# Kernel optimization log

Hardware: AMD Instinct MI355X
Metric: run time of the kernel (lower is better)

The kernel has to match this reference:

```python
import jax, jax.numpy as jnp
import numpy as np

L = 2        # rnn_num_layer
H = 512      # rnn_hidden_size
E = 512      # embed_dim == rnn_input_size
B = 16
T_DEC = 512
S_ENC = 512
VOCAB = 1001 # num_embed
OUT = 1000   # output_size
PAD = 0.0


def setup_inputs() -> dict:
    key = jax.random.key(0)
    ks = jax.random.split(key, 16)
    s = 0.05
    trg_inputs = jax.random.randint(ks[0], (B, T_DEC), 0, VOCAB)
    trg_len = jnp.clip(jax.random.randint(ks[1], (B,), 0, T_DEC + 1), 1, T_DEC)
    encoder_outputs = jax.random.normal(ks[2], (B, S_ENC, H), dtype=jnp.float32)
    h0 = jax.random.normal(ks[3], (L * 2, B, H), dtype=jnp.float32)
    c0 = jax.random.normal(ks[4], (L * 2, B, H), dtype=jnp.float32)
    embed = jax.random.normal(ks[5], (VOCAB, E)) * s
    W_ih0 = jax.random.normal(ks[6], (2, 4 * H, E)) * s          # layer 0, fwd/bwd dirs
    W_ih1 = jax.random.normal(ks[7], (L - 1, 2, 4 * H, 2 * H)) * s  # layers>0 take concat(fwd,bwd)
    W_hh = jax.random.normal(ks[8], (L, 2, 4 * H, H)) * s
    b_ih = jax.random.normal(ks[9], (L, 2, 4 * H)) * s
    b_hh = jax.random.normal(ks[10], (L, 2, 4 * H)) * s
    W_att = jax.random.normal(ks[11], (H, H)) * s  # Attention 'general' linear
    b_att = jax.random.normal(ks[12], (H,)) * s
    W_fc = jax.random.normal(ks[13], (OUT, 2 * H)) * s
    b_fc = jax.random.normal(ks[14], (OUT,)) * s
    return dict(trg_inputs=trg_inputs, trg_len=trg_len, encoder_outputs=encoder_outputs,
                h0=h0, c0=c0, embed=embed, W_ih0=W_ih0, W_ih1=W_ih1, W_hh=W_hh,
                b_ih=b_ih, b_hh=b_hh, W_att=W_att, b_att=b_att, W_fc=W_fc, b_fc=b_fc)


def _cell(x, h, c, Wi, Wh, bi, bh):
    # PyTorch LSTM gate order: i, f, g, o
    g = x @ Wi.T + h @ Wh.T + bi + bh  # [B, 4H]
    i, f, gg, o = jnp.split(g, 4, axis=-1)
    c2 = jax.nn.sigmoid(f) * c + jax.nn.sigmoid(i) * jnp.tanh(gg)
    h2 = jax.nn.sigmoid(o) * jnp.tanh(c2)
    return h2, c2


def _decode(trg_inputs, trg_len, encoder_outputs, h0, c0, embed,
            W_ih0, W_ih1, W_hh, b_ih, b_hh, W_att, b_att, W_fc, b_fc):
    Bb, T = trg_inputs.shape
    S = encoder_outputs.shape[1]
    # 'general' attention projection of encoder outputs (hoisted out of the loop)
    enc_proj = jnp.einsum('bsh,gh->bsg', encoder_outputs, W_att) + b_att
    enc_mask = jnp.arange(S)[None, :] < trg_len[:, None]          # [B, S]
    step_valid = jnp.arange(T)[:, None] < trg_len[None, :]        # [T, B]
    h = h0.reshape(L, 2, Bb, H)
    c = c0.reshape(L, 2, Bb, H)

    def step(carry, xt):
        h, c = carry
        tok, valid = xt                                           # [B], [B]
        xin = embed[tok]                                          # [B, E]
        hs, cs = [], []
        for l in range(L):
            Wi = W_ih0 if l == 0 else W_ih1[l - 1]
            hf, cf = _cell(xin, h[l, 0], c[l, 0], Wi[0], W_hh[l, 0], b_ih[l, 0], b_hh[l, 0])
            hb, cb = _cell(xin, h[l, 1], c[l, 1], Wi[1], W_hh[l, 1], b_ih[l, 1], b_hh[l, 1])
            hs.append(jnp.stack([hf, hb]))
            cs.append(jnp.stack([cf, cb]))
            xin = jnp.concatenate([hf, hb], axis=-1)              # input to next layer [B, 2H]
        h2 = jnp.stack(hs)
        c2 = jnp.stack(cs)
        dec = hs[-1][0] + hs[-1][1]                               # sum fwd+bwd halves [B, H]
        score = jnp.einsum('bh,bsh->bs', dec, enc_proj)
        score = jnp.where(enc_mask, score, -1e30)                 # ragged length mask
        att = jax.nn.softmax(score, axis=-1)
        ctx = jnp.einsum('bs,bsh->bh', att, encoder_outputs)
        fc = jnp.concatenate([dec, ctx], axis=-1) @ W_fc.T + b_fc # [B, OUT]
        out = jnp.where(valid[:, None], fc, PAD)                  # positions past trg_len stay pad
        return (h2, c2), out

    _, outs = jax.lax.scan(step, (h, c), (trg_inputs.T, step_valid))
    return outs.transpose(1, 0, 2)                                # [B, T, OUT]


def reference(trg_inputs, trg_len, encoder_outputs, h0, c0, embed,
              W_ih0, W_ih1, W_hh, b_ih, b_hh, W_att, b_att, W_fc, b_fc):
    return _decode(trg_inputs, trg_len, encoder_outputs, h0, c0, embed,
                   W_ih0, W_ih1, W_hh, b_ih, b_hh, W_att, b_att, W_fc, b_fc)
```

## Files before the change

kernel.cpp:

```cpp
#include <hip/hip_runtime.h>
#include <cstdint>
#include <cstddef>

typedef __attribute__((ext_vector_type(8))) short short8;
typedef __attribute__((ext_vector_type(4))) float f32x4;
typedef __attribute__((ext_vector_type(4))) unsigned int uint4v;

#define DEV static __device__ __forceinline__

DEV float b2f(unsigned short u){ union{unsigned int i; float f;} v; v.i = ((unsigned int)u)<<16; return v.f; }
DEV unsigned short f2b(float f){
  union{float f; unsigned int i;} v; v.f = f;
  unsigned int u = v.i;
  unsigned int r = (u + 0x7fffu + ((u>>16)&1u)) >> 16;
  return (unsigned short)r;
}
DEV float sigm(float x){ return 1.0f/(1.0f + __expf(-x)); }
DEV float tanhfast(float x){ return 1.0f - 2.0f/(1.0f + __expf(2.0f*x)); }

DEV uint4v ld_sc_b128(const unsigned short* p){
  uint4v d;
  asm volatile("global_load_dwordx4 %0, %1, off sc0 sc1" : "=v"(d) : "v"(p) : "memory");
  return d;
}
DEV short8 ldw8(const float* p){
  short8 w;
  #pragma unroll
  for (int e = 0; e < 8; ++e) w[e] = (short)f2b(p[e]);
  return w;
}

__global__ __launch_bounds__(256) void k_cast(const float* __restrict__ s, unsigned short* __restrict__ d, int n){
  int i = blockIdx.x*256 + threadIdx.x;
  if (i < n) d[i] = f2b(s[i]);
}
__global__ __launch_bounds__(256) void k_transpose_enc(const float* __restrict__ enc, unsigned short* __restrict__ encT){
  int i = blockIdx.x*256 + threadIdx.x;
  if (i >= 16*512*512) return;
  int b = i >> 18, r = i & 262143, h = r >> 9, s = r & 511;
  encT[i] = f2b(enc[(b<<18) + (s<<9) + h]);
}
__global__ __launch_bounds__(256) void k_gather(const int* __restrict__ trg, const float* __restrict__ emb, unsigned short* __restrict__ X){
  int i = blockIdx.x*256 + threadIdx.x;
  if (i >= 8192*512) return;
  int r = i >> 9, e = i & 511;
  int t = r >> 4, b = r & 15;
  int tok = trg[(b<<9) + t];
  X[i] = f2b(emb[((size_t)tok<<9) + e]);
}
__global__ __launch_bounds__(256) void k_bsum(const float* __restrict__ bi, const float* __restrict__ bh, float* __restrict__ o){
  int i = blockIdx.x*256 + threadIdx.x;
  if (i < 8192) o[i] = bi[i] + bh[i];
}
__global__ __launch_bounds__(256) void k_init(const float* __restrict__ h0, unsigned short* __restrict__ Hst0,
                                              unsigned short* __restrict__ Hst1, unsigned int* __restrict__ bar){
  int i = blockIdx.x*256 + threadIdx.x;
  if (i < 256) bar[i] = 0;
  if (i < 16384) {
    Hst0[i] = f2b(h0[i]);
    Hst1[i] = f2b(h0[16384 + i]);
  }
}
__global__ __launch_bounds__(256) void k_split(const float* __restrict__ S, unsigned short* __restrict__ E3, int n){
  int i = blockIdx.x*256 + threadIdx.x;
  if (i >= n) return;
  int r = i >> 9, j = i & 511;
  float f = S[i];
  unsigned short hi = f2b(f);
  unsigned short lo = f2b(f - b2f(hi));
  size_t base = (size_t)r * 1536 + j;
  E3[base] = hi;
  E3[base + 512] = lo;
  E3[base + 1024] = hi;
}
__global__ __launch_bounds__(256) void k_decsplit(const float* __restrict__ HF, unsigned short* __restrict__ DCTX,
                                                  unsigned short* __restrict__ D3){
  int i = blockIdx.x*256 + threadIdx.x;
  if (i >= 8192*512) return;
  int r = i >> 9, j = i & 511;
  float d = HF[((size_t)r<<10) + j] + HF[((size_t)r<<10) + 512 + j];
  unsigned short hi = f2b(d);
  unsigned short lo = f2b(d - b2f(hi));
  DCTX[((size_t)r<<10) + j] = hi;
  size_t base = (size_t)r * 1536 + j;
  D3[base] = hi;
  D3[base + 512] = hi;
  D3[base + 1024] = lo;
}

template<int MODE>
__global__ __launch_bounds__(256) void k_gemm(
    const unsigned short* __restrict__ A, long lda, long sA,
    const unsigned short* __restrict__ W, long ldw, long sW,
    void* __restrict__ C, long ldc, long sC,
    const float* __restrict__ bias,
    int M, int N, int K,
    const int* __restrict__ tlen)
{
  __shared__ short8 AsV[128*5];
  __shared__ short8 WsV[128*5];
  const int bz = blockIdx.z;
  const unsigned short* Ab = A + (size_t)bz * sA;
  const unsigned short* Wb = W + (size_t)bz * sW;
  const int m0 = blockIdx.x << 7, n0 = blockIdx.y << 7;
  const int tid = threadIdx.x;
  const int wave = tid >> 6, lane = tid & 63;
  const int ln = lane & 15, kq = lane >> 4;
  const int wm = wave >> 1, wn = wave & 1;
  const int ar0 = tid >> 2, ac0 = (tid & 3) << 3;
  const int ar1 = ar0 + 64;
  const short8 z8 = {0,0,0,0,0,0,0,0};

  f32x4 acc[4][4];
  #pragma unroll
  for (int i = 0; i < 4; ++i)
    #pragma unroll
    for (int j = 0; j < 4; ++j) { f32x4 z = {0.f,0.f,0.f,0.f}; acc[i][j] = z; }

  for (int k0 = 0; k0 < K; k0 += 32) {
    short8 a0 = *(const short8*)(Ab + (size_t)(m0+ar0)*lda + k0 + ac0);
    short8 a1 = *(const short8*)(Ab + (size_t)(m0+ar1)*lda + k0 + ac0);
    short8 w0 = z8, w1 = z8;
    if (MODE != 2 || (n0+ar0) < N) w0 = *(const short8*)(Wb + (size_t)(n0+ar0)*ldw + k0 + ac0);
    if (MODE != 2 || (n0+ar1) < N) w1 = *(const short8*)(Wb + (size_t)(n0+ar1)*ldw + k0 + ac0);
    __syncthreads();
    AsV[ar0*5 + (ac0>>3)] = a0;
    AsV[ar1*5 + (ac0>>3)] = a1;
    WsV[ar0*5 + (ac0>>3)] = w0;
    WsV[ar1*5 + (ac0>>3)] = w1;
    __syncthreads();
    short8 af[4], wf[4];
    #pragma unroll
    for (int i = 0; i < 4; ++i) af[i] = AsV[((wm<<6) + (i<<4) + ln)*5 + kq];
    #pragma unroll
    for (int i = 0; i < 4; ++i) wf[i] = WsV[((wn<<6) + (i<<4) + ln)*5 + kq];
    #pragma unroll
    for (int i = 0; i < 4; ++i)
      #pragma unroll
      for (int j = 0; j < 4; ++j)
        acc[i][j] = __builtin_amdgcn_mfma_f32_16x16x32_bf16(af[i], wf[j], acc[i][j], 0, 0, 0);
  }
  #pragma unroll
  for (int j = 0; j < 4; ++j) {
    const int n = n0 + (wn<<6) + (j<<4) + ln;
    float bi = 0.f;
    if (MODE == 0 || MODE == 1) { if (bias) bi = bias[n]; }
    if (MODE == 2) { if (n < N) bi = bias[n]; }
    #pragma unroll
    for (int i = 0; i < 4; ++i) {
      #pragma unroll
      for (int r = 0; r < 4; ++r) {
        const int m = m0 + (wm<<6) + (i<<4) + (kq<<2) + r;
        float v = acc[i][j][r] + bi;
        if (MODE == 0) ((unsigned short*)C)[(size_t)bz*sC + (size_t)m*ldc + n] = f2b(v);
        else if (MODE == 1) ((float*)C)[(size_t)bz*sC + (size_t)m*ldc + n] = v;
        else {
          if (n < N) {
            int tt = m >> 4, bb = m & 15;
            ((float*)C)[((size_t)((bb<<9) + tt))*1000 + n] = (tt < tlen[bb]) ? v : 0.0f;
          }
        }
      }
    }
  }
}

__global__ __launch_bounds__(256, 1) void k_recur(
    const float* __restrict__ whh,
    const float* __restrict__ wih1,
    const unsigned short* __restrict__ Xg0,
    const float* __restrict__ c0all,
    const float* __restrict__ bsum,
    unsigned short* __restrict__ Hst0,
    unsigned short* __restrict__ Hst1,
    unsigned short* __restrict__ Hcat,
    float* __restrict__ HcatF,
    unsigned int* __restrict__ flags)
{
  const int bid = blockIdx.x;
  const int dir = (bid >> 5) & 1;
  const int j0  = (bid & 31) << 4;
  const int tid = threadIdx.x;
  const int wave = tid >> 6, lane = tid & 63;
  const int ln = lane & 15, kq = lane >> 4;
  const int b_ = tid >> 4, jl = tid & 15;
  const int myfl = bid & 31, pollfl = lane & 31;

  __shared__ __align__(16) unsigned char h0sh[32768];
  __shared__ __align__(16) unsigned char h1sh[16384];
  __shared__ float gsh[4][16][16];

  unsigned int* FL0d0 = flags;
  unsigned int* FL0d1 = flags + 32;

  if (bid < 64) {
    unsigned int* FL = flags + (dir << 5);
    short8 wfrag[16];
    {
      const float* wb = whh + (((size_t)((dir<<11) + (wave<<9) + j0 + ln)) << 9) + (kq<<3);
      #pragma unroll
      for (int ks = 0; ks < 16; ++ks) wfrag[ks] = ldw8(wb + (ks<<5));
    }
    float c = c0all[(((size_t)((dir<<4) + b_)) << 9) + j0 + jl];

    size_t xr = ((size_t)b_ << 12) + (dir<<11) + j0 + jl;
    float xg0 = b2f(Xg0[xr]);
    float xg1 = b2f(Xg0[xr + 512]);
    float xg2 = b2f(Xg0[xr + 1024]);
    float xg3 = b2f(Xg0[xr + 1536]);

    for (int t = 0; t < 512; ++t) {
      const unsigned short* hbase = Hst0 + ((((t&1)<<1) + dir)<<13);
      uint4v st[4];
      #pragma unroll
      for (int cc = 0; cc < 4; ++cc)
        st[cc] = ld_sc_b128(hbase + (cc<<11) + (tid<<3));
      asm volatile("s_waitcnt vmcnt(0)" ::: "memory");
      #pragma unroll
      for (int cc = 0; cc < 4; ++cc) {
        int g = (cc<<8) + tid, row = g >> 6, slot = g & 63, ps = slot ^ row;
        *(uint4v*)(h1sh + row*1024 + (ps<<4)) = st[cc];
      }
      __syncthreads();

      f32x4 acc0 = {0.f,0.f,0.f,0.f}, acc1 = {0.f,0.f,0.f,0.f};
      #pragma unroll
      for (int ks = 0; ks < 16; ks += 2) {
        short8 a0 = *(const short8*)(h1sh + ln*1024 + ((((ks<<2)+kq) ^ ln)<<4));
        short8 a1 = *(const short8*)(h1sh + ln*1024 + (((((ks+1)<<2)+kq) ^ ln)<<4));
        acc0 = __builtin_amdgcn_mfma_f32_16x16x32_bf16(a0, wfrag[ks],   acc0, 0, 0, 0);
        acc1 = __builtin_amdgcn_mfma_f32_16x16x32_bf16(a1, wfrag[ks+1], acc1, 0, 0, 0);
      }
      f32x4 acc = acc0 + acc1;
      #pragma unroll
      for (int r = 0; r < 4; ++r)
        gsh[wave][(kq<<2)+r][ln] = acc[r];
      __syncthreads();

      float gi = gsh[0][b_][jl] + xg0;
      float gf = gsh[1][b_][jl] + xg1;
      float gg = gsh[2][b_][jl] + xg2;
      float go = gsh[3][b_][jl] + xg3;
      float ii = sigm(gi), ff = sigm(gf);
      float g2 = tanhfast(gg), oo = sigm(go);
      c = ff*c + ii*g2;
      float h = oo * tanhfast(c);
      unsigned short h16 = f2b(h);

      unsigned int hu = (unsigned int)h16;
      unsigned int hv1 = __shfl_down(hu, 1);
      unsigned int hv2 = __shfl_down(hu, 2);
      unsigned int hv3 = __shfl_down(hu, 3);
      if (!(lane & 3)) {
        unsigned long long hq = (unsigned long long)(hu | (hv1 << 16))
                              | ((unsigned long long)(hv2 | (hv3 << 16)) << 32);
        unsigned short* dst = Hst0 + (((((t+1)&1)<<1) + dir)<<13) + (b_<<9) + j0 + jl;
        __hip_atomic_store((unsigned long long*)dst, hq, __ATOMIC_RELAXED, __HIP_MEMORY_SCOPE_AGENT);
        unsigned short* dc = Hcat + (((size_t)((t<<4) + b_))<<10) + (dir<<9) + j0 + jl;
        __hip_atomic_store((unsigned long long*)dc, hq, __ATOMIC_RELAXED, __HIP_MEMORY_SCOPE_AGENT);
      }

      if (t < 511) {
        xr = (((size_t)(((t+1)<<4) + b_)) << 12) + (dir<<11) + j0 + jl;
        xg0 = b2f(Xg0[xr]);
        xg1 = b2f(Xg0[xr + 512]);
        xg2 = b2f(Xg0[xr + 1024]);
        xg3 = b2f(Xg0[xr + 1536]);
      }

      __syncthreads();
      if (tid == 0)
        __hip_atomic_store(FL + myfl, (unsigned int)(t + 1), __ATOMIC_RELAXED, __HIP_MEMORY_SCOPE_AGENT);
      if (t == 511) break;

      if (wave == 0) {
        const unsigned int tgt = (unsigned int)(t + 1);
        while (!__all((int)(__hip_atomic_load(FL + pollfl, __ATOMIC_RELAXED, __HIP_MEMORY_SCOPE_AGENT) >= tgt)))
          __builtin_amdgcn_s_sleep(1);
      }
      __syncthreads();
    }
  } else {
    unsigned int* FL = flags + 64 + (dir << 5);
    short8 whf[16];
    {
      const float* wb = whh + 2097152 + (((size_t)((dir<<11) + (wave<<9) + j0 + ln)) << 9) + (kq<<3);
      #pragma unroll
      for (int ks = 0; ks < 16; ++ks) whf[ks] = ldw8(wb + (ks<<5));
    }
    short8 wxf[32];
    {
      const float* xb = wih1 + (((size_t)((dir<<11) + (wave<<9) + j0 + ln)) << 10) + (kq<<3);
      #pragma unroll
      for (int ks = 0; ks < 32; ++ks) wxf[ks] = ldw8(xb + (ks<<5));
    }
    float c = c0all[16384 + (((size_t)((dir<<4) + b_)) << 9) + j0 + jl];
    float bs0 = bsum[4096 + (dir<<11) + 0*512 + j0 + jl];
    float bs1 = bsum[4096 + (dir<<11) + 1*512 + j0 + jl];
    float bs2 = bsum[4096 + (dir<<11) + 2*512 + j0 + jl];
    float bs3 = bsum[4096 + (dir<<11) + 3*512 + j0 + jl];

    if (wave == 0) {
      const unsigned int* fp = (lane < 32) ? (FL0d0 + lane) : (FL0d1 + (lane - 32));
      while (!__all((int)(__hip_atomic_load(fp, __ATOMIC_RELAXED, __HIP_MEMORY_SCOPE_AGENT) >= 2u)))
        __builtin_amdgcn_s_sleep(1);
    }
    __syncthreads();

    uint4v sxr[8];
    #pragma unroll
    for (int cc = 0; cc < 8; ++cc) {
      int g = (cc<<8) + tid, row = g >> 7, slot = g & 127;
      sxr[cc] = ld_sc_b128(Hcat + (row<<10) + (slot<<3));
    }
    asm volatile("s_waitcnt vmcnt(0)" ::: "memory");
    #pragma unroll
    for (int cc = 0; cc < 8; ++cc) {
      int g = (cc<<8) + tid, row = g >> 7, slot = g & 127, ps = slot ^ row;
      *(uint4v*)(h0sh + row*2048 + (ps<<4)) = sxr[cc];
    }
    __syncthreads();
    f32x4 xacc;
    {
      f32x4 xa = {0.f,0.f,0.f,0.f}, xb2 = {0.f,0.f,0.f,0.f};
      #pragma unroll
      for (int ks = 0; ks < 32; ks += 2) {
        short8 a0 = *(const short8*)(h0sh + ln*2048 + ((((ks<<2)+kq) ^ ln)<<4));
        short8 a1 = *(const short8*)(h0sh + ln*2048 + (((((ks+1)<<2)+kq) ^ ln)<<4));
        xa  = __builtin_amdgcn_mfma_f32_16x16x32_bf16(a0, wxf[ks],   xa, 0, 0, 0);
        xb2 = __builtin_amdgcn_mfma_f32_16x16x32_bf16(a1, wxf[ks+1], xb2, 0, 0, 0);
      }
      xacc = xa + xb2;
    }
    #pragma unroll
    for (int cc = 0; cc < 8; ++cc) {
      int g = (cc<<8) + tid, row = g >> 7, slot = g & 127;
      sxr[cc] = ld_sc_b128(Hcat + 16384 + (row<<10) + (slot<<3));
    }

    for (int t = 0; t < 512; ++t) {
      if (wave == 0) {
        const unsigned int tgt = (unsigned int)t;
        if (t > 0)
          while (!__all((int)(__hip_atomic_load(FL + pollfl, __ATOMIC_RELAXED, __HIP_MEMORY_SCOPE_AGENT) >= tgt)))
            __builtin_amdgcn_s_sleep(1);
      } else if (wave == 1) {
        const unsigned int tgt = (t + 3 < 512) ? (unsigned int)(t + 3) : 512u;
        const unsigned int* fp = (lane < 32) ? (FL0d0 + lane) : (FL0d1 + (lane - 32));
        while (!__all((int)(__hip_atomic_load(fp, __ATOMIC_RELAXED, __HIP_MEMORY_SCOPE_AGENT) >= tgt)))
          __builtin_amdgcn_s_sleep(1);
      }
      __syncthreads();

      const unsigned short* h1base = Hst1 + ((((t&1)<<1) + dir)<<13);
      uint4v sh[4];
      #pragma unroll
      for (int cc = 0; cc < 4; ++cc)
        sh[cc] = ld_sc_b128(h1base + (cc<<11) + (tid<<3));
      asm volatile("s_waitcnt vmcnt(0)" ::: "memory");
      #pragma unroll
      for (int cc = 0; cc < 4; ++cc) {
        int g = (cc<<8) + tid, row = g >> 6, slot = g & 63, ps = slot ^ row;
        *(uint4v*)(h1sh + row*1024 + (ps<<4)) = sh[cc];
      }
      __syncthreads();

      f32x4 acc0 = xacc, acc1 = {0.f,0.f,0.f,0.f};
      #pragma unroll
      for (int ks = 0; ks < 16; ks += 2) {
        short8 a0 = *(const short8*)(h1sh + ln*1024 + ((((ks<<2)+kq) ^ ln)<<4));
        short8 a1 = *(const short8*)(h1sh + ln*1024 + (((((ks+1)<<2)+kq) ^ ln)<<4));
        acc0 = __builtin_amdgcn_mfma_f32_16x16x32_bf16(a0, whf[ks],   acc0, 0, 0, 0);
        acc1 = __builtin_amdgcn_mfma_f32_16x16x32_bf16(a1, whf[ks+1], acc1, 0, 0, 0);
      }
      f32x4 acc = acc0 + acc1;
      #pragma unroll
      for (int r = 0; r < 4; ++r)
        gsh[wave][(kq<<2)+r][ln] = acc[r];
      __syncthreads();

      float gi = gsh[0][b_][jl] + bs0;
      float gf = gsh[1][b_][jl] + bs1;
      float gg = gsh[2][b_][jl] + bs2;
      float go = gsh[3][b_][jl] + bs3;
      float ii = sigm(gi), ff = sigm(gf);
      float g2 = tanhfast(gg), oo = sigm(go);
      c = ff*c + ii*g2;
      float h = oo * tanhfast(c);
      unsigned short h16 = f2b(h);

      unsigned int hu = (unsigned int)h16;
      unsigned int hv1 = __shfl_down(hu, 1);
      unsigned int hv2 = __shfl_down(hu, 2);
      unsigned int hv3 = __shfl_down(hu, 3);
      if (!(lane & 3)) {
        unsigned long long hq = (unsigned long long)(hu | (hv1 << 16))
                              | ((unsigned long long)(hv2 | (hv3 << 16)) << 32);
        unsigned short* dst = Hst1 + (((((t+1)&1)<<1) + dir)<<13) + (b_<<9) + j0 + jl;
        __hip_atomic_store((unsigned long long*)dst, hq, __ATOMIC_RELAXED, __HIP_MEMORY_SCOPE_AGENT);
      }

      __syncthreads();
      if (tid == 0)
        __hip_atomic_store(FL + myfl, (unsigned int)(t + 1), __ATOMIC_RELAXED, __HIP_MEMORY_SCOPE_AGENT);

      __builtin_nontemporal_store(h, HcatF + (((size_t)((t<<4) + b_))<<10) + (dir<<9) + j0 + jl);

      if (t == 511) break;

      #pragma unroll
      for (int cc = 0; cc < 8; ++cc) {
        int g = (cc<<8) + tid, row = g >> 7, slot = g & 127, ps = slot ^ row;
        *(uint4v*)(h0sh + row*2048 + (ps<<4)) = sxr[cc];
      }
      __syncthreads();
      {
        f32x4 xa = {0.f,0.f,0.f,0.f}, xb2 = {0.f,0.f,0.f,0.f};
        #pragma unroll
        for (int ks = 0; ks < 32; ks += 2) {
          short8 a0 = *(const short8*)(h0sh + ln*2048 + ((((ks<<2)+kq) ^ ln)<<4));
          short8 a1 = *(const short8*)(h0sh + ln*2048 + (((((ks+1)<<2)+kq) ^ ln)<<4));
          xa  = __builtin_amdgcn_mfma_f32_16x16x32_bf16(a0, wxf[ks],   xa, 0, 0, 0);
          xb2 = __builtin_amdgcn_mfma_f32_16x16x32_bf16(a1, wxf[ks+1], xb2, 0, 0, 0);
        }
        xacc = xa + xb2;
      }
      if (t < 510) {
        const unsigned short* hb0 = Hcat + (((size_t)(t+2)) << 14);
        #pragma unroll
        for (int cc = 0; cc < 8; ++cc) {
          int g = (cc<<8) + tid, row = g >> 7, slot = g & 127;
          sxr[cc] = ld_sc_b128(hb0 + (row<<10) + (slot<<3));
        }
      }
    }
  }
}

__global__ __launch_bounds__(256) void k_softmax(const float* __restrict__ score, const int* __restrict__ tlen,
                                                 unsigned short* __restrict__ att){
  int row = (blockIdx.x<<2) + (threadIdx.x>>6);
  int lane = threadIdx.x & 63;
  int b = row >> 9;
  int len = tlen[b];
  const float* sr = score + ((size_t)row<<9);
  float v[8]; float m = -3.0e38f;
  #pragma unroll
  for (int i = 0; i < 8; ++i) {
    int s = (i<<6) + lane;
    float x = sr[s];
    v[i] = (s < len) ? x : -1.0e30f;
    m = fmaxf(m, v[i]);
  }
  #pragma unroll
  for (int off = 32; off; off >>= 1) m = fmaxf(m, __shfl_xor(m, off));
  float sum = 0.f; float p[8];
  #pragma unroll
  for (int i = 0; i < 8; ++i) { p[i] = __expf(v[i] - m); sum += p[i]; }
  #pragma unroll
  for (int off = 32; off; off >>= 1) sum += __shfl_xor(sum, off);
  float inv = 1.0f / sum;
  unsigned short* ar = att + ((size_t)row<<9);
  #pragma unroll
  for (int i = 0; i < 8; ++i) ar[(i<<6) + lane] = f2b(p[i]*inv);
}

extern "C" void kernel_launch(void* const* d_in, const int* in_sizes, int n_in,
                              void* d_out, int out_size, void* d_ws, size_t ws_size,
                              hipStream_t stream) {
  (void)in_sizes; (void)n_in; (void)out_size; (void)ws_size;
  const int*   trg  = (const int*)d_in[0];
  const int*   tlen = (const int*)d_in[1];
  const float* enc  = (const float*)d_in[2];
  const float* h0   = (const float*)d_in[3];
  const float* c0   = (const float*)d_in[4];
  const float* emb  = (const float*)d_in[5];
  const float* wih0 = (const float*)d_in[6];
  const float* wih1 = (const float*)d_in[7];
  const float* whh  = (const float*)d_in[8];
  const float* bih  = (const float*)d_in[9];
  const float* bhh  = (const float*)d_in[10];
  const float* watt = (const float*)d_in[11];
  const float* batt = (const float*)d_in[12];
  const float* wfc  = (const float*)d_in[13];
  const float* bfc  = (const float*)d_in[14];
  float* out = (float*)d_out;

  char* ws = (char*)d_ws;
  size_t off = 0;
  auto alloc = [&](size_t bytes)->char* {
    char* p = ws + off; off += (bytes + 255) & ~(size_t)255; return p;
  };
  unsigned int*   BAR   = (unsigned int*)  alloc(1024);
  unsigned short* XEMB  = (unsigned short*)alloc(8192ll*512*2);
  unsigned short* WI0B  = (unsigned short*)alloc(4096ll*512*2);
  unsigned short* WFCB  = (unsigned short*)alloc(1000ll*1024*2);
  unsigned short* WATTB = (unsigned short*)alloc(512ll*512*2);
  unsigned short* ENCB  = (unsigned short*)alloc(8192ll*512*2);
  unsigned short* ENCT  = (unsigned short*)alloc(8192ll*512*2);
  float*          BSUM  = (float*)         alloc(8192*4);
  unsigned short* HST0  = (unsigned short*)alloc(32768*2);
  unsigned short* HST1  = (unsigned short*)alloc(32768*2);
  unsigned short* XG    = (unsigned short*)alloc(8192ll*4096*2);
  unsigned short* HCAT  = (unsigned short*)alloc(8192ll*1024*2);
  float*          HCATF = (float*)         alloc(8192ll*1024*4);
  float*          SCORE = (float*)         alloc(8192ll*512*4);
  unsigned short* ATT   = (unsigned short*)alloc(8192ll*512*2);
  unsigned short* DCTX  = (unsigned short*)alloc(8192ll*1024*2);
  unsigned short* DEC3  = XG;
  unsigned short* ENC3  = XG + 8192ll*1536;

  auto cdiv = [](long a, long b){ return (int)((a + b - 1) / b); };

  k_cast<<<cdiv(2097152,256),256,0,stream>>>(wih0, WI0B, 2097152);
  k_cast<<<cdiv(1024000,256),256,0,stream>>>(wfc,  WFCB, 1024000);
  k_cast<<<cdiv(262144,256),256,0,stream>>>(watt, WATTB, 262144);
  k_cast<<<cdiv(4194304,256),256,0,stream>>>(enc,  ENCB, 4194304);
  k_transpose_enc<<<cdiv(4194304,256),256,0,stream>>>(enc, ENCT);
  k_gather<<<cdiv(4194304,256),256,0,stream>>>(trg, emb, XEMB);
  k_bsum<<<cdiv(8192,256),256,0,stream>>>(bih, bhh, BSUM);
  k_init<<<cdiv(32768,256),256,0,stream>>>(h0, HST0, HST1, BAR);

  k_gemm<1><<<dim3(64,4,1),256,0,stream>>>(ENCB,512,0, WATTB,512,0, (void*)SCORE,512,0, batt, 8192,512,512, nullptr);

  k_gemm<0><<<dim3(64,32,1),256,0,stream>>>(XEMB,512,0, WI0B,512,0, (void*)XG,4096,0, BSUM, 8192,4096,512, nullptr);

  k_recur<<<128,256,0,stream>>>(whh, wih1, XG, c0, BSUM, HST0, HST1, HCAT, HCATF, BAR);

  k_split<<<cdiv(4194304,256),256,0,stream>>>(SCORE, ENC3, 4194304);
  k_decsplit<<<cdiv(4194304,256),256,0,stream>>>(HCATF, DCTX, DEC3);

  k_gemm<1><<<dim3(4,4,16),256,0,stream>>>(DEC3,24576,1536, ENC3,1536,786432, (void*)SCORE,512,262144, nullptr, 512,512,1536, nullptr);

  k_softmax<<<2048,256,0,stream>>>(SCORE, tlen, ATT);

  k_gemm<0><<<dim3(4,4,16),256,0,stream>>>(ATT,512,262144, ENCT,512,262144, (void*)(DCTX+512),16384,1024, nullptr, 512,512,512, nullptr);

  k_gemm<2><<<dim3(64,8,1),256,0,stream>>>(DCTX,1024,0, WFCB,1024,0, (void*)out,1000,0, bfc, 8192,1000,1024, tlen);
}
```

Before: 1.846 ms.

## Split layer-1 recurrence into recurrent and input-projection wave groups

Doubles the recurrent kernel's block size to 512 threads. In layer-1 blocks, waves 4-7 compute the next step's input projection from layer-0 outputs into a double-buffered shared array. Meanwhile waves 0-3 run the hidden-state matmul and the gate math, which takes the input projection off the serial critical path. Layer-0 blocks get extra idle waves that only help with the state load. This adds register and shared-memory pressure, extra barriers, and changed flag-wait thresholds.

```diff
diff --git a/kernel.cpp b/kernel.cpp
--- a/kernel.cpp
+++ b/kernel.cpp
@@ -165,7 +165,7 @@
   }
 }
 
-__global__ __launch_bounds__(256, 1) void k_recur(
+__global__ __launch_bounds__(512, 1) void k_recur(
     const float* __restrict__ whh,
     const float* __restrict__ wih1,
     const unsigned short* __restrict__ Xg0,
@@ -183,12 +183,13 @@
   const int tid = threadIdx.x;
   const int wave = tid >> 6, lane = tid & 63;
   const int ln = lane & 15, kq = lane >> 4;
-  const int b_ = tid >> 4, jl = tid & 15;
+  const int b_ = (tid & 255) >> 4, jl = tid & 15;
   const int myfl = bid & 31, pollfl = lane & 31;
 
   __shared__ __align__(16) unsigned char h0sh[32768];
   __shared__ __align__(16) unsigned char h1sh[16384];
   __shared__ float gsh[4][16][16];
+  __shared__ float gshX[2][4][16][16];
 
   unsigned int* FL0d0 = flags;
   unsigned int* FL0d1 = flags + 32;
@@ -196,76 +197,82 @@
   if (bid < 64) {
     unsigned int* FL = flags + (dir << 5);
     short8 wfrag[16];
-    {
+    if (wave < 4) {
       const float* wb = whh + (((size_t)((dir<<11) + (wave<<9) + j0 + ln)) << 9) + (kq<<3);
       #pragma unroll
       for (int ks = 0; ks < 16; ++ks) wfrag[ks] = ldw8(wb + (ks<<5));
     }
-    float c = c0all[(((size_t)((dir<<4) + b_)) << 9) + j0 + jl];
-
-    size_t xr = ((size_t)b_ << 12) + (dir<<11) + j0 + jl;
-    float xg0 = b2f(Xg0[xr]);
-    float xg1 = b2f(Xg0[xr + 512]);
-    float xg2 = b2f(Xg0[xr + 1024]);
-    float xg3 = b2f(Xg0[xr + 1536]);
+    float c = 0.f, xg0 = 0.f, xg1 = 0.f, xg2 = 0.f, xg3 = 0.f;
+    if (tid < 256) {
+      c = c0all[(((size_t)((dir<<4) + b_)) << 9) + j0 + jl];
+      size_t xr = ((size_t)b_ << 12) + (dir<<11) + j0 + jl;
+      xg0 = b2f(Xg0[xr]);
+      xg1 = b2f(Xg0[xr + 512]);
+      xg2 = b2f(Xg0[xr + 1024]);
+      xg3 = b2f(Xg0[xr + 1536]);
+    }
 
     for (int t = 0; t < 512; ++t) {
       const unsigned short* hbase = Hst0 + ((((t&1)<<1) + dir)<<13);
-      uint4v st[4];
-      #pragma unroll
-      for (int cc = 0; cc < 4; ++cc)
-        st[cc] = ld_sc_b128(hbase + (cc<<11) + (tid<<3));
+      uint4v st[2];
+      #pragma unroll
+      for (int cc = 0; cc < 2; ++cc)
+        st[cc] = ld_sc_b128(hbase + (cc<<12) + (tid<<3));
       asm volatile("s_waitcnt vmcnt(0)" ::: "memory");
       #pragma unroll
-      for (int cc = 0; cc < 4; ++cc) {
-        int g = (cc<<8) + tid, row = g >> 6, slot = g & 63, ps = slot ^ row;
+      for (int cc = 0; cc < 2; ++cc) {
+        int g = (cc<<9) + tid, row = g >> 6, slot = g & 63, ps = slot ^ row;
         *(uint4v*)(h1sh + row*1024 + (ps<<4)) = st[cc];
       }
       __syncthreads();
 
-      f32x4 acc0 = {0.f,0.f,0.f,0.f}, acc1 = {0.f,0.f,0.f,0.f};
-      #pragma unroll
-      for (int ks = 0; ks < 16; ks += 2) {
-        short8 a0 = *(const short8*)(h1sh + ln*1024 + ((((ks<<2)+kq) ^ ln)<<4));
-        short8 a1 = *(const short8*)(h1sh + ln*1024 + (((((ks+1)<<2)+kq) ^ ln)<<4));
-        acc0 = __builtin_amdgcn_mfma_f32_16x16x32_bf16(a0, wfrag[ks],   acc0, 0, 0, 0);
-        acc1 = __builtin_amdgcn_mfma_f32_16x16x32_bf16(a1, wfrag[ks+1], acc1, 0, 0, 0);
-      }
-      f32x4 acc = acc0 + acc1;
-      #pragma unroll
-      for (int r = 0; r < 4; ++r)
-        gsh[wave][(kq<<2)+r][ln] = acc[r];
-      __syncthreads();
-
-      float gi = gsh[0][b_][jl] + xg0;
-      float gf = gsh[1][b_][jl] + xg1;
-      float gg = gsh[2][b_][jl] + xg2;
-      float go = gsh[3][b_][jl] + xg3;
-      float ii = sigm(gi), ff = sigm(gf);
-      float g2 = tanhfast(gg), oo = sigm(go);
-      c = ff*c + ii*g2;
-      float h = oo * tanhfast(c);
-      unsigned short h16 = f2b(h);
-
-      unsigned int hu = (unsigned int)h16;
-      unsigned int hv1 = __shfl_down(hu, 1);
-      unsigned int hv2 = __shfl_down(hu, 2);
-      unsigned int hv3 = __shfl_down(hu, 3);
-      if (!(lane & 3)) {
-        unsigned long long hq = (unsigned long long)(hu | (hv1 << 16))
-                              | ((unsigned long long)(hv2 | (hv3 << 16)) << 32);
-        unsigned short* dst = Hst0 + (((((t+1)&1)<<1) + dir)<<13) + (b_<<9) + j0 + jl;
-        __hip_atomic_store((unsigned long long*)dst, hq, __ATOMIC_RELAXED, __HIP_MEMORY_SCOPE_AGENT);
-        unsigned short* dc = Hcat + (((size_t)((t<<4) + b_))<<10) + (dir<<9) + j0 + jl;
-        __hip_atomic_store((unsigned long long*)dc, hq, __ATOMIC_RELAXED, __HIP_MEMORY_SCOPE_AGENT);
-      }
-
-      if (t < 511) {
-        xr = (((size_t)(((t+1)<<4) + b_)) << 12) + (dir<<11) + j0 + jl;
-        xg0 = b2f(Xg0[xr]);
-        xg1 = b2f(Xg0[xr + 512]);
-        xg2 = b2f(Xg0[xr + 1024]);
-        xg3 = b2f(Xg0[xr + 1536]);
+      if (tid < 256) {
+        f32x4 acc0 = {0.f,0.f,0.f,0.f}, acc1 = {0.f,0.f,0.f,0.f};
+        #pragma unroll
+        for (int ks = 0; ks < 16; ks += 2) {
+          short8 a0 = *(const short8*)(h1sh + ln*1024 + ((((ks<<2)+kq) ^ ln)<<4));
+          short8 a1 = *(const short8*)(h1sh + ln*1024 + (((((ks+1)<<2)+kq) ^ ln)<<4));
+          acc0 = __builtin_amdgcn_mfma_f32_16x16x32_bf16(a0, wfrag[ks],   acc0, 0, 0, 0);
+          acc1 = __builtin_amdgcn_mfma_f32_16x16x32_bf16(a1, wfrag[ks+1], acc1, 0, 0, 0);
+        }
+        f32x4 acc = acc0 + acc1;
+        #pragma unroll
+        for (int r = 0; r < 4; ++r)
+          gsh[wave][(kq<<2)+r][ln] = acc[r];
+      }
+      __syncthreads();
+
+      if (tid < 256) {
+        float gi = gsh[0][b_][jl] + xg0;
+        float gf = gsh[1][b_][jl] + xg1;
+        float gg = gsh[2][b_][jl] + xg2;
+        float go = gsh[3][b_][jl] + xg3;
+        float ii = sigm(gi), ff = sigm(gf);
+        float g2 = tanhfast(gg), oo = sigm(go);
+        c = ff*c + ii*g2;
+        float h = oo * tanhfast(c);
+        unsigned short h16 = f2b(h);
+
+        unsigned int hu = (unsigned int)h16;
+        unsigned int hv1 = __shfl_down(hu, 1);
+        unsigned int hv2 = __shfl_down(hu, 2);
+        unsigned int hv3 = __shfl_down(hu, 3);
+        if (!(lane & 3)) {
+          unsigned long long hq = (unsigned long long)(hu | (hv1 << 16))
+                                | ((unsigned long long)(hv2 | (hv3 << 16)) << 32);
+          unsigned short* dst = Hst0 + (((((t+1)&1)<<1) + dir)<<13) + (b_<<9) + j0 + jl;
+          __hip_atomic_store((unsigned long long*)dst, hq, __ATOMIC_RELAXED, __HIP_MEMORY_SCOPE_AGENT);
+          unsigned short* dc = Hcat + (((size_t)((t<<4) + b_))<<10) + (dir<<9) + j0 + jl;
+          __hip_atomic_store((unsigned long long*)dc, hq, __ATOMIC_RELAXED, __HIP_MEMORY_SCOPE_AGENT);
+        }
+
+        if (t < 511) {
+          size_t xr = (((size_t)(((t+1)<<4) + b_)) << 12) + (dir<<11) + j0 + jl;
+          xg0 = b2f(Xg0[xr]);
+          xg1 = b2f(Xg0[xr + 512]);
+          xg2 = b2f(Xg0[xr + 1024]);
+          xg3 = b2f(Xg0[xr + 1536]);
+        }
       }
 
       __syncthreads();
@@ -282,46 +289,50 @@
     }
   } else {
     unsigned int* FL = flags + 64 + (dir << 5);
+    const int xq = (wave >= 4) ? (wave - 4) : 0;
+    const int xtid = tid & 255;
     short8 whf[16];
-    {
+    short8 wxf[32];
+    if (wave < 4) {
       const float* wb = whh + 2097152 + (((size_t)((dir<<11) + (wave<<9) + j0 + ln)) << 9) + (kq<<3);
       #pragma unroll
       for (int ks = 0; ks < 16; ++ks) whf[ks] = ldw8(wb + (ks<<5));
-    }
-    short8 wxf[32];
-    {
-      const float* xb = wih1 + (((size_t)((dir<<11) + (wave<<9) + j0 + ln)) << 10) + (kq<<3);
+    } else {
+      const float* xb = wih1 + (((size_t)((dir<<11) + (xq<<9) + j0 + ln)) << 10) + (kq<<3);
       #pragma unroll
       for (int ks = 0; ks < 32; ++ks) wxf[ks] = ldw8(xb + (ks<<5));
     }
-    float c = c0all[16384 + (((size_t)((dir<<4) + b_)) << 9) + j0 + jl];
-    float bs0 = bsum[4096 + (dir<<11) + 0*512 + j0 + jl];
-    float bs1 = bsum[4096 + (dir<<11) + 1*512 + j0 + jl];
-    float bs2 = bsum[4096 + (dir<<11) + 2*512 + j0 + jl];
-    float bs3 = bsum[4096 + (dir<<11) + 3*512 + j0 + jl];
-
-    if (wave == 0) {
+    float c = 0.f, bs0 = 0.f, bs1 = 0.f, bs2 = 0.f, bs3 = 0.f;
+    if (tid < 256) {
+      c = c0all[16384 + (((size_t)((dir<<4) + b_)) << 9) + j0 + jl];
+      bs0 = bsum[4096 + (dir<<11) + 0*512 + j0 + jl];
+      bs1 = bsum[4096 + (dir<<11) + 1*512 + j0 + jl];
+      bs2 = bsum[4096 + (dir<<11) + 2*512 + j0 + jl];
+      bs3 = bsum[4096 + (dir<<11) + 3*512 + j0 + jl];
+    }
+
+    if (wave == 4) {
       const unsigned int* fp = (lane < 32) ? (FL0d0 + lane) : (FL0d1 + (lane - 32));
-      while (!__all((int)(__hip_atomic_load(fp, __ATOMIC_RELAXED, __HIP_MEMORY_SCOPE_AGENT) >= 2u)))
+      while (!__all((int)(__hip_atomic_load(fp, __ATOMIC_RELAXED, __HIP_MEMORY_SCOPE_AGENT) >= 1u)))
         __builtin_amdgcn_s_sleep(1);
     }
     __syncthreads();
-
-    uint4v sxr[8];
-    #pragma unroll
-    for (int cc = 0; cc < 8; ++cc) {
-      int g = (cc<<8) + tid, row = g >> 7, slot = g & 127;
-      sxr[cc] = ld_sc_b128(Hcat + (row<<10) + (slot<<3));
-    }
-    asm volatile("s_waitcnt vmcnt(0)" ::: "memory");
-    #pragma unroll
-    for (int cc = 0; cc < 8; ++cc) {
-      int g = (cc<<8) + tid, row = g >> 7, slot = g & 127, ps = slot ^ row;
-      *(uint4v*)(h0sh + row*2048 + (ps<<4)) = sxr[cc];
+    if (wave >= 4) {
+      uint4v sx[8];
+      #pragma unroll
+      for (int cc = 0; cc < 8; ++cc) {
+        int g = (cc<<8) + xtid, row = g >> 7, slot = g & 127;
+        sx[cc] = ld_sc_b128(Hcat + (row<<10) + (slot<<3));
+      }
+      asm volatile("s_waitcnt vmcnt(0)" ::: "memory");
+      #pragma unroll
+      for (int cc = 0; cc < 8; ++cc) {
+        int g = (cc<<8) + xtid, row = g >> 7, slot = g & 127, ps = slot ^ row;
+        *(uint4v*)(h0sh + row*2048 + (ps<<4)) = sx[cc];
+      }
     }
     __syncthreads();
-    f32x4 xacc;
-    {
+    if (wave >= 4) {
       f32x4 xa = {0.f,0.f,0.f,0.f}, xb2 = {0.f,0.f,0.f,0.f};
       #pragma unroll
       for (int ks = 0; ks < 32; ks += 2) {
@@ -330,91 +341,95 @@
         xa  = __builtin_amdgcn_mfma_f32_16x16x32_bf16(a0, wxf[ks],   xa, 0, 0, 0);
         xb2 = __builtin_amdgcn_mfma_f32_16x16x32_bf16(a1, wxf[ks+1], xb2, 0, 0, 0);
       }
-      xacc = xa + xb2;
-    }
-    #pragma unroll
-    for (int cc = 0; cc < 8; ++cc) {
-      int g = (cc<<8) + tid, row = g >> 7, slot = g & 127;
-      sxr[cc] = ld_sc_b128(Hcat + 16384 + (row<<10) + (slot<<3));
+      f32x4 x = xa + xb2;
+      #pragma unroll
+      for (int r = 0; r < 4; ++r)
+        gshX[0][xq][(kq<<2)+r][ln] = x[r];
     }
 
     for (int t = 0; t < 512; ++t) {
       if (wave == 0) {
-        const unsigned int tgt = (unsigned int)t;
-        if (t > 0)
+        if (t > 0) {
+          const unsigned int tgt = (unsigned int)t;
           while (!__all((int)(__hip_atomic_load(FL + pollfl, __ATOMIC_RELAXED, __HIP_MEMORY_SCOPE_AGENT) >= tgt)))
             __builtin_amdgcn_s_sleep(1);
-      } else if (wave == 1) {
-        const unsigned int tgt = (t + 3 < 512) ? (unsigned int)(t + 3) : 512u;
+        }
+      } else if (wave == 4) {
+        const unsigned int tgt = (t + 2 < 512) ? (unsigned int)(t + 2) : 512u;
         const unsigned int* fp = (lane < 32) ? (FL0d0 + lane) : (FL0d1 + (lane - 32));
         while (!__all((int)(__hip_atomic_load(fp, __ATOMIC_RELAXED, __HIP_MEMORY_SCOPE_AGENT) >= tgt)))
           __builtin_amdgcn_s_sleep(1);
       }
       __syncthreads();
 
-      const unsigned short* h1base = Hst1 + ((((t&1)<<1) + dir)<<13);
-      uint4v sh[4];
-      #pragma unroll
-      for (int cc = 0; cc < 4; ++cc)
-        sh[cc] = ld_sc_b128(h1base + (cc<<11) + (tid<<3));
-      asm volatile("s_waitcnt vmcnt(0)" ::: "memory");
-      #pragma unroll
-      for (int cc = 0; cc < 4; ++cc) {
-        int g = (cc<<8) + tid, row = g >> 6, slot = g & 63, ps = slot ^ row;
-        *(uint4v*)(h1sh + row*1024 + (ps<<4)) = sh[cc];
-      }
-      __syncthreads();
-
-      f32x4 acc0 = xacc, acc1 = {0.f,0.f,0.f,0.f};
-      #pragma unroll
-      for (int ks = 0; ks < 16; ks += 2) {
-        short8 a0 = *(const short8*)(h1sh + ln*1024 + ((((ks<<2)+kq) ^ ln)<<4));
-        short8 a1 = *(const short8*)(h1sh + ln*1024 + (((((ks+1)<<2)+kq) ^ ln)<<4));
-        acc0 = __builtin_amdgcn_mfma_f32_16x16x32_bf16(a0, whf[ks],   acc0, 0, 0, 0);
-        acc1 = __builtin_amdgcn_mfma_f32_16x16x32_bf16(a1, whf[ks+1], acc1, 0, 0, 0);
-      }
-      f32x4 acc = acc0 + acc1;
-      #pragma unroll
-      for (int r = 0; r < 4; ++r)
-        gsh[wave][(kq<<2)+r][ln] = acc[r];
-      __syncthreads();
-
-      float gi = gsh[0][b_][jl] + bs0;
-      float gf = gsh[1][b_][jl] + bs1;
-      float gg = gsh[2][b_][jl] + bs2;
-      float go = gsh[3][b_][jl] + bs3;
-      float ii = sigm(gi), ff = sigm(gf);
-      float g2 = tanhfast(gg), oo = sigm(go);
-      c = ff*c + ii*g2;
-      float h = oo * tanhfast(c);
-      unsigned short h16 = f2b(h);
-
-      unsigned int hu = (unsigned int)h16;
-      unsigned int hv1 = __shfl_down(hu, 1);
-      unsigned int hv2 = __shfl_down(hu, 2);
-      unsigned int hv3 = __shfl_down(hu, 3);
-      if (!(lane & 3)) {
-        unsigned long long hq = (unsigned long long)(hu | (hv1 << 16))
-                              | ((unsigned long long)(hv2 | (hv3 << 16)) << 32);
-        unsigned short* dst = Hst1 + (((((t+1)&1)<<1) + dir)<<13) + (b_<<9) + j0 + jl;
-        __hip_atomic_store((unsigned long long*)dst, hq, __ATOMIC_RELAXED, __HIP_MEMORY_SCOPE_AGENT);
-      }
-
-      __syncthreads();
-      if (tid == 0)
-        __hip_atomic_store(FL + myfl, (unsigned int)(t + 1), __ATOMIC_RELAXED, __HIP_MEMORY_SCOPE_AGENT);
-
-      __builtin_nontemporal_store(h, HcatF + (((size_t)((t<<4) + b_))<<10) + (dir<<9) + j0 + jl);
-
-      if (t == 511) break;
-
-      #pragma unroll
-      for (int cc = 0; cc < 8; ++cc) {
-        int g = (cc<<8) + tid, row = g >> 7, slot = g & 127, ps = slot ^ row;
-        *(uint4v*)(h0sh + row*2048 + (ps<<4)) = sxr[cc];
-      }
-      __syncthreads();
-      {
+      if (wave < 4) {
+        const unsigned short* h1base = Hst1 + ((((t&1)<<1) + dir)<<13);
+        uint4v sh[4];
+        #pragma unroll
+        for (int cc = 0; cc < 4; ++cc)
+          sh[cc] = ld_sc_b128(h1base + (cc<<11) + (tid<<3));
+        asm volatile("s_waitcnt vmcnt(0)" ::: "memory");
+        #pragma unroll
+        for (int cc = 0; cc < 4; ++cc) {
+          int g = (cc<<8) + tid, row = g >> 6, slot = g & 63, ps = slot ^ row;
+          *(uint4v*)(h1sh + row*1024 + (ps<<4)) = sh[cc];
+        }
+      } else if (t < 511) {
+        const unsigned short* h0base = Hcat + (((size_t)(t+1)) << 14);
+        uint4v sx[8];
+        #pragma unroll
+        for (int cc = 0; cc < 8; ++cc) {
+          int g = (cc<<8) + xtid, row = g >> 7, slot = g & 127;
+          sx[cc] = ld_sc_b128(h0base + (row<<10) + (slot<<3));
+        }
+        asm volatile("s_waitcnt vmcnt(0)" ::: "memory");
+        #pragma unroll
+        for (int cc = 0; cc < 8; ++cc) {
+          int g = (cc<<8) + xtid, row = g >> 7, slot = g & 127, ps = slot ^ row;
+          *(uint4v*)(h0sh + row*2048 + (ps<<4)) = sx[cc];
+        }
+      }
+      __syncthreads();
+
+      if (wave < 4) {
+        f32x4 acc0 = {0.f,0.f,0.f,0.f}, acc1 = {0.f,0.f,0.f,0.f};
+        #pragma unroll
+        for (int ks = 0; ks < 16; ks += 2) {
+          short8 a0 = *(const short8*)(h1sh + ln*1024 + ((((ks<<2)+kq) ^ ln)<<4));
+          short8 a1 = *(const short8*)(h1sh + ln*1024 + (((((ks+1)<<2)+kq) ^ ln)<<4));
+          acc0 = __builtin_amdgcn_mfma_f32_16x16x32_bf16(a0, whf[ks],   acc0, 0, 0, 0);
+          acc1 = __builtin_amdgcn_mfma_f32_16x16x32_bf16(a1, whf[ks+1], acc1, 0, 0, 0);
+        }
+        f32x4 acc = acc0 + acc1;
+        #pragma unroll
+        for (int r = 0; r < 4; ++r)
+          gsh[wave][(kq<<2)+r][ln] = acc[r];
+      }
+      __syncthreads();
+
+      if (tid < 256) {
+        float gi = gsh[0][b_][jl] + gshX[t&1][0][b_][jl] + bs0;
+        float gf = gsh[1][b_][jl] + gshX[t&1][1][b_][jl] + bs1;
+        float gg = gsh[2][b_][jl] + gshX[t&1][2][b_][jl] + bs2;
+        float go = gsh[3][b_][jl] + gshX[t&1][3][b_][jl] + bs3;
+        float ii = sigm(gi), ff = sigm(gf);
+        float g2 = tanhfast(gg), oo = sigm(go);
+        c = ff*c + ii*g2;
+        float h = oo * tanhfast(c);
+        unsigned short h16 = f2b(h);
+
+        unsigned int hu = (unsigned int)h16;
+        unsigned int hv1 = __shfl_down(hu, 1);
+        unsigned int hv2 = __shfl_down(hu, 2);
+        unsigned int hv3 = __shfl_down(hu, 3);
+        if (!(lane & 3)) {
+          unsigned long long hq = (unsigned long long)(hu | (hv1 << 16))
+                                | ((unsigned long long)(hv2 | (hv3 << 16)) << 32);
+          unsigned short* dst = Hst1 + (((((t+1)&1)<<1) + dir)<<13) + (b_<<9) + j0 + jl;
+          __hip_atomic_store((unsigned long long*)dst, hq, __ATOMIC_RELAXED, __HIP_MEMORY_SCOPE_AGENT);
+        }
+        __builtin_nontemporal_store(h, HcatF + (((size_t)((t<<4) + b_))<<10) + (dir<<9) + j0 + jl);
+      } else if (t < 511) {
         f32x4 xa = {0.f,0.f,0.f,0.f}, xb2 = {0.f,0.f,0.f,0.f};
         #pragma unroll
         for (int ks = 0; ks < 32; ks += 2) {
@@ -423,16 +438,15 @@
           xa  = __builtin_amdgcn_mfma_f32_16x16x32_bf16(a0, wxf[ks],   xa, 0, 0, 0);
           xb2 = __builtin_amdgcn_mfma_f32_16x16x32_bf16(a1, wxf[ks+1], xb2, 0, 0, 0);
         }
-        xacc = xa + xb2;
-      }
-      if (t < 510) {
-        const unsigned short* hb0 = Hcat + (((size_t)(t+2)) << 14);
-        #pragma unroll
-        for (int cc = 0; cc < 8; ++cc) {
-          int g = (cc<<8) + tid, row = g >> 7, slot = g & 127;
-          sxr[cc] = ld_sc_b128(hb0 + (row<<10) + (slot<<3));
-        }
-      }
+        f32x4 x = xa + xb2;
+        #pragma unroll
+        for (int r = 0; r < 4; ++r)
+          gshX[(t+1)&1][xq][(kq<<2)+r][ln] = x[r];
+      }
+
+      __syncthreads();
+      if (tid == 0)
+        __hip_atomic_store(FL + myfl, (unsigned int)(t + 1), __ATOMIC_RELAXED, __HIP_MEMORY_SCOPE_AGENT);
     }
   }
 }
@@ -525,7 +539,7 @@
 
   k_gemm<0><<<dim3(64,32,1),256,0,stream>>>(XEMB,512,0, WI0B,512,0, (void*)XG,4096,0, BSUM, 8192,4096,512, nullptr);
 
-  k_recur<<<128,256,0,stream>>>(whh, wih1, XG, c0, BSUM, HST0, HST1, HCAT, HCATF, BAR);
+  k_recur<<<128,512,0,stream>>>(whh, wih1, XG, c0, BSUM, HST0, HST1, HCAT, HCATF, BAR);
 
   k_split<<<cdiv(4194304,256),256,0,stream>>>(SCORE, ENC3, 4194304);
   k_decsplit<<<cdiv(4194304,256),256,0,stream>>>(HCATF, DCTX, DEC3);
```

New measurement: 2.906 ms. 57.4% more time.

## Split layer-1 input projection into separate producer blocks with ring buffer

Applied to the files above, without the earlier changes.

Adds 64 extra blocks to the persistent recurrence kernel that compute the layer-1 input-gate projection (W_ih1 · concat(h_fwd, h_bwd)) for each timestep. They publish the results into an 8-slot fp32 ring buffer guarded by new flags. The layer-1 recurrence blocks no longer hold W_ih1 in registers or run that projection on their critical path; they just load the precomputed gates each step. The aim is to shorten each layer-1 step and free registers, at the cost of an extra flag wait per step, more global traffic, and 192 co-resident blocks needed for the spin-wait scheme to stay deadlock-free.

```diff
diff --git a/kernel.cpp b/kernel.cpp
--- a/kernel.cpp
+++ b/kernel.cpp
@@ -175,6 +175,7 @@
     unsigned short* __restrict__ Hst1,
     unsigned short* __restrict__ Hcat,
     float* __restrict__ HcatF,
+    float* __restrict__ XG1,
     unsigned int* __restrict__ flags)
 {
   const int bid = blockIdx.x;
@@ -280,19 +281,14 @@
       }
       __syncthreads();
     }
-  } else {
-    unsigned int* FL = flags + 64 + (dir << 5);
+  } else if (bid < 128) {
+    unsigned int* FL  = flags + 64 + (dir << 5);
+    unsigned int* FXP = flags + 128 + (dir << 5);
     short8 whf[16];
     {
       const float* wb = whh + 2097152 + (((size_t)((dir<<11) + (wave<<9) + j0 + ln)) << 9) + (kq<<3);
       #pragma unroll
       for (int ks = 0; ks < 16; ++ks) whf[ks] = ldw8(wb + (ks<<5));
-    }
-    short8 wxf[32];
-    {
-      const float* xb = wih1 + (((size_t)((dir<<11) + (wave<<9) + j0 + ln)) << 10) + (kq<<3);
-      #pragma unroll
-      for (int ks = 0; ks < 32; ++ks) wxf[ks] = ldw8(xb + (ks<<5));
     }
     float c = c0all[16384 + (((size_t)((dir<<4) + b_)) << 9) + j0 + jl];
     float bs0 = bsum[4096 + (dir<<11) + 0*512 + j0 + jl];
@@ -300,54 +296,16 @@
     float bs2 = bsum[4096 + (dir<<11) + 2*512 + j0 + jl];
     float bs3 = bsum[4096 + (dir<<11) + 3*512 + j0 + jl];
 
-    if (wave == 0) {
-      const unsigned int* fp = (lane < 32) ? (FL0d0 + lane) : (FL0d1 + (lane - 32));
-      while (!__all((int)(__hip_atomic_load(fp, __ATOMIC_RELAXED, __HIP_MEMORY_SCOPE_AGENT) >= 2u)))
-        __builtin_amdgcn_s_sleep(1);
-    }
-    __syncthreads();
-
-    uint4v sxr[8];
-    #pragma unroll
-    for (int cc = 0; cc < 8; ++cc) {
-      int g = (cc<<8) + tid, row = g >> 7, slot = g & 127;
-      sxr[cc] = ld_sc_b128(Hcat + (row<<10) + (slot<<3));
-    }
-    asm volatile("s_waitcnt vmcnt(0)" ::: "memory");
-    #pragma unroll
-    for (int cc = 0; cc < 8; ++cc) {
-      int g = (cc<<8) + tid, row = g >> 7, slot = g & 127, ps = slot ^ row;
-      *(uint4v*)(h0sh + row*2048 + (ps<<4)) = sxr[cc];
-    }
-    __syncthreads();
-    f32x4 xacc;
-    {
-      f32x4 xa = {0.f,0.f,0.f,0.f}, xb2 = {0.f,0.f,0.f,0.f};
-      #pragma unroll
-      for (int ks = 0; ks < 32; ks += 2) {
-        short8 a0 = *(const short8*)(h0sh + ln*2048 + ((((ks<<2)+kq) ^ ln)<<4));
-        short8 a1 = *(const short8*)(h0sh + ln*2048 + (((((ks+1)<<2)+kq) ^ ln)<<4));
-        xa  = __builtin_amdgcn_mfma_f32_16x16x32_bf16(a0, wxf[ks],   xa, 0, 0, 0);
-        xb2 = __builtin_amdgcn_mfma_f32_16x16x32_bf16(a1, wxf[ks+1], xb2, 0, 0, 0);
-      }
-      xacc = xa + xb2;
-    }
-    #pragma unroll
-    for (int cc = 0; cc < 8; ++cc) {
-      int g = (cc<<8) + tid, row = g >> 7, slot = g & 127;
-      sxr[cc] = ld_sc_b128(Hcat + 16384 + (row<<10) + (slot<<3));
-    }
-
     for (int t = 0; t < 512; ++t) {
       if (wave == 0) {
-        const unsigned int tgt = (unsigned int)t;
-        if (t > 0)
+        if (t > 0) {
+          const unsigned int tgt = (unsigned int)t;
           while (!__all((int)(__hip_atomic_load(FL + pollfl, __ATOMIC_RELAXED, __HIP_MEMORY_SCOPE_AGENT) >= tgt)))
             __builtin_amdgcn_s_sleep(1);
+        }
       } else if (wave == 1) {
-        const unsigned int tgt = (t + 3 < 512) ? (unsigned int)(t + 3) : 512u;
-        const unsigned int* fp = (lane < 32) ? (FL0d0 + lane) : (FL0d1 + (lane - 32));
-        while (!__all((int)(__hip_atomic_load(fp, __ATOMIC_RELAXED, __HIP_MEMORY_SCOPE_AGENT) >= tgt)))
+        const unsigned int tgt = (unsigned int)(t + 1);
+        while (!__all((int)(__hip_atomic_load(FXP + pollfl, __ATOMIC_RELAXED, __HIP_MEMORY_SCOPE_AGENT) >= tgt)))
           __builtin_amdgcn_s_sleep(1);
       }
       __syncthreads();
@@ -357,6 +315,8 @@
       #pragma unroll
       for (int cc = 0; cc < 4; ++cc)
         sh[cc] = ld_sc_b128(h1base + (cc<<11) + (tid<<3));
+      const float* xp = XG1 + ((((size_t)((((t&7)<<1) + dir)<<4) + b_)<<9) + j0 + jl)*4;
+      uint4v xgu = ld_sc_b128((const unsigned short*)xp);
       asm volatile("s_waitcnt vmcnt(0)" ::: "memory");
       #pragma unroll
       for (int cc = 0; cc < 4; ++cc) {
@@ -365,7 +325,7 @@
       }
       __syncthreads();
 
-      f32x4 acc0 = xacc, acc1 = {0.f,0.f,0.f,0.f};
+      f32x4 acc0 = {0.f,0.f,0.f,0.f}, acc1 = {0.f,0.f,0.f,0.f};
       #pragma unroll
       for (int ks = 0; ks < 16; ks += 2) {
         short8 a0 = *(const short8*)(h1sh + ln*1024 + ((((ks<<2)+kq) ^ ln)<<4));
@@ -379,10 +339,11 @@
         gsh[wave][(kq<<2)+r][ln] = acc[r];
       __syncthreads();
 
-      float gi = gsh[0][b_][jl] + bs0;
-      float gf = gsh[1][b_][jl] + bs1;
-      float gg = gsh[2][b_][jl] + bs2;
-      float go = gsh[3][b_][jl] + bs3;
+      union { uint4v u; f32x4 f; } xg; xg.u = xgu;
+      float gi = gsh[0][b_][jl] + xg.f[0] + bs0;
+      float gf = gsh[1][b_][jl] + xg.f[1] + bs1;
+      float gg = gsh[2][b_][jl] + xg.f[2] + bs2;
+      float go = gsh[3][b_][jl] + xg.f[3] + bs3;
       float ii = sigm(gi), ff = sigm(gf);
       float g2 = tanhfast(gg), oo = sigm(go);
       c = ff*c + ii*g2;
@@ -399,40 +360,78 @@
         unsigned short* dst = Hst1 + (((((t+1)&1)<<1) + dir)<<13) + (b_<<9) + j0 + jl;
         __hip_atomic_store((unsigned long long*)dst, hq, __ATOMIC_RELAXED, __HIP_MEMORY_SCOPE_AGENT);
       }
+      __builtin_nontemporal_store(h, HcatF + (((size_t)((t<<4) + b_))<<10) + (dir<<9) + j0 + jl);
 
       __syncthreads();
       if (tid == 0)
         __hip_atomic_store(FL + myfl, (unsigned int)(t + 1), __ATOMIC_RELAXED, __HIP_MEMORY_SCOPE_AGENT);
-
-      __builtin_nontemporal_store(h, HcatF + (((size_t)((t<<4) + b_))<<10) + (dir<<9) + j0 + jl);
-
-      if (t == 511) break;
-
+    }
+  } else {
+    unsigned int* FXP = flags + 128 + (dir << 5);
+    unsigned int* FL1 = flags + 64  + (dir << 5);
+    short8 wxf[32];
+    {
+      const float* xb = wih1 + (((size_t)((dir<<11) + (wave<<9) + j0 + ln)) << 10) + (kq<<3);
+      #pragma unroll
+      for (int ks = 0; ks < 32; ++ks) wxf[ks] = ldw8(xb + (ks<<5));
+    }
+
+    for (int t = 0; t < 512; ++t) {
+      if (wave == 0) {
+        const unsigned int tgt = (unsigned int)(t + 1);
+        const unsigned int* fp = (lane < 32) ? (FL0d0 + lane) : (FL0d1 + (lane - 32));
+        while (!__all((int)(__hip_atomic_load(fp, __ATOMIC_RELAXED, __HIP_MEMORY_SCOPE_AGENT) >= tgt)))
+          __builtin_amdgcn_s_sleep(1);
+      } else if (wave == 1 && t >= 8) {
+        const unsigned int tgt = (unsigned int)(t - 7);
+        while (!__all((int)(__hip_atomic_load(FL1 + pollfl, __ATOMIC_RELAXED, __HIP_MEMORY_SCOPE_AGENT) >= tgt)))
+          __builtin_amdgcn_s_sleep(1);
+      }
+      __syncthreads();
+
+      const unsigned short* h0base = Hcat + (((size_t)t) << 14);
+      uint4v sx[8];
+      #pragma unroll
+      for (int cc = 0; cc < 8; ++cc) {
+        int g = (cc<<8) + tid, row = g >> 7, slot = g & 127;
+        sx[cc] = ld_sc_b128(h0base + (row<<10) + (slot<<3));
+      }
+      asm volatile("s_waitcnt vmcnt(0)" ::: "memory");
       #pragma unroll
       for (int cc = 0; cc < 8; ++cc) {
         int g = (cc<<8) + tid, row = g >> 7, slot = g & 127, ps = slot ^ row;
-        *(uint4v*)(h0sh + row*2048 + (ps<<4)) = sxr[cc];
-      }
-      __syncthreads();
+        *(uint4v*)(h0sh + row*2048 + (ps<<4)) = sx[cc];
+      }
+      __syncthreads();
+
+      f32x4 xa = {0.f,0.f,0.f,0.f}, xb2 = {0.f,0.f,0.f,0.f};
+      #pragma unroll
+      for (int ks = 0; ks < 32; ks += 2) {
+        short8 a0 = *(const short8*)(h0sh + ln*2048 + ((((ks<<2)+kq) ^ ln)<<4));
+        short8 a1 = *(const short8*)(h0sh + ln*2048 + (((((ks+1)<<2)+kq) ^ ln)<<4));
+        xa  = __builtin_amdgcn_mfma_f32_16x16x32_bf16(a0, wxf[ks],   xa, 0, 0, 0);
+        xb2 = __builtin_amdgcn_mfma_f32_16x16x32_bf16(a1, wxf[ks+1], xb2, 0, 0, 0);
+      }
+      f32x4 x = xa + xb2;
+      #pragma unroll
+      for (int r = 0; r < 4; ++r)
+        gsh[wave][(kq<<2)+r][ln] = x[r];
+      __syncthreads();
+
       {
-        f32x4 xa = {0.f,0.f,0.f,0.f}, xb2 = {0.f,0.f,0.f,0.f};
-        #pragma unroll
-        for (int ks = 0; ks < 32; ks += 2) {
-          short8 a0 = *(const short8*)(h0sh + ln*2048 + ((((ks<<2)+kq) ^ ln)<<4));
-          short8 a1 = *(const short8*)(h0sh + ln*2048 + (((((ks+1)<<2)+kq) ^ ln)<<4));
-          xa  = __builtin_amdgcn_mfma_f32_16x16x32_bf16(a0, wxf[ks],   xa, 0, 0, 0);
-          xb2 = __builtin_amdgcn_mfma_f32_16x16x32_bf16(a1, wxf[ks+1], xb2, 0, 0, 0);
-        }
-        xacc = xa + xb2;
-      }
-      if (t < 510) {
-        const unsigned short* hb0 = Hcat + (((size_t)(t+2)) << 14);
-        #pragma unroll
-        for (int cc = 0; cc < 8; ++cc) {
-          int g = (cc<<8) + tid, row = g >> 7, slot = g & 127;
-          sxr[cc] = ld_sc_b128(hb0 + (row<<10) + (slot<<3));
-        }
-      }
+        union { f32x4 f; unsigned long long u[2]; } xg;
+        xg.f[0] = gsh[0][b_][jl];
+        xg.f[1] = gsh[1][b_][jl];
+        xg.f[2] = gsh[2][b_][jl];
+        xg.f[3] = gsh[3][b_][jl];
+        float* dst = XG1 + ((((size_t)((((t&7)<<1) + dir)<<4) + b_)<<9) + j0 + jl)*4;
+        __hip_atomic_store((unsigned long long*)dst,       xg.u[0], __ATOMIC_RELAXED, __HIP_MEMORY_SCOPE_AGENT);
+        __hip_atomic_store(((unsigned long long*)dst) + 1, xg.u[1], __ATOMIC_RELAXED, __HIP_MEMORY_SCOPE_AGENT);
+      }
+
+      __syncthreads();
+      if (tid == 0)
+        __hip_atomic_store(FXP + myfl, (unsigned int)(t + 1), __ATOMIC_RELAXED, __HIP_MEMORY_SCOPE_AGENT);
     }
   }
 }
@@ -492,6 +491,7 @@
     char* p = ws + off; off += (bytes + 255) & ~(size_t)255; return p;
   };
   unsigned int*   BAR   = (unsigned int*)  alloc(1024);
+  float*          XG1   = (float*)         alloc(8ll*2*16*512*4*4);
   unsigned short* XEMB  = (unsigned short*)alloc(8192ll*512*2);
   unsigned short* WI0B  = (unsigned short*)alloc(4096ll*512*2);
   unsigned short* WFCB  = (unsigned short*)alloc(1000ll*1024*2);
@@ -525,7 +525,7 @@
 
   k_gemm<0><<<dim3(64,32,1),256,0,stream>>>(XEMB,512,0, WI0B,512,0, (void*)XG,4096,0, BSUM, 8192,4096,512, nullptr);
 
-  k_recur<<<128,256,0,stream>>>(whh, wih1, XG, c0, BSUM, HST0, HST1, HCAT, HCATF, BAR);
+  k_recur<<<192,256,0,stream>>>(whh, wih1, XG, c0, BSUM, HST0, HST1, HCAT, HCATF, XG1, BAR);
 
   k_split<<<cdiv(4194304,256),256,0,stream>>>(SCORE, ENC3, 4194304);
   k_decsplit<<<cdiv(4194304,256),256,0,stream>>>(HCATF, DCTX, DEC3);
```

Result: slower. 1.938 ms (+5.0%).
